# Kernel tuning notes

Measured on AMD Instinct MI355X. Metric: run time of the kernel, lower is better.

The kernel has to match this reference:

```python
import jax, jax.numpy as jnp
import numpy as np

H = 1024        # hidden_units
NH = 16         # num_heads
HD = H // NH    # head_dim = 64
B = 32
S = 500
MAX_SEQ = 500
ROPE_BASE = 10000.0


def setup_inputs() -> dict:
    key = jax.random.key(0)
    ks = jax.random.split(key, 16)
    s = 1.0 / np.sqrt(H)
    inp = {
        "query": jax.random.normal(ks[0], (B, S, H), jnp.float32),
        "key":   jax.random.normal(ks[1], (B, S, H), jnp.float32),
        "value": jax.random.normal(ks[2], (B, S, H), jnp.float32),
        "attn_mask": jax.random.randint(ks[3], (B, S), 0, 2).astype(bool),
        "Wq": jax.random.uniform(ks[4], (H, H), jnp.float32, -s, s),
        "bq": jax.random.uniform(ks[5], (H,), jnp.float32, -s, s),
        "Wk": jax.random.uniform(ks[6], (H, H), jnp.float32, -s, s),
        "bk": jax.random.uniform(ks[7], (H,), jnp.float32, -s, s),
        "Wv": jax.random.uniform(ks[8], (H, H), jnp.float32, -s, s),
        "bv": jax.random.uniform(ks[9], (H,), jnp.float32, -s, s),
        "Wo": jax.random.uniform(ks[10], (H, H), jnp.float32, -s, s),
        "bo": jax.random.uniform(ks[11], (H,), jnp.float32, -s, s),
        # rel_pos_bias embedding table: [2*max_seq_len-1, num_heads]
        "rel_emb": jax.random.normal(ks[12], (2 * MAX_SEQ - 1, NH), jnp.float32),
    }
    return inp


def _rope_tables(seq_len, head_dim, dtype):
    inv_freq = 1.0 / (ROPE_BASE ** (jnp.arange(0, head_dim, 2, dtype=jnp.float32) / head_dim))
    t = jnp.arange(seq_len, dtype=jnp.float32)
    freqs = t[:, None] * inv_freq[None, :]           # [S, HD/2]
    emb = jnp.concatenate([freqs, freqs], axis=-1)   # [S, HD]
    return jnp.cos(emb).astype(dtype), jnp.sin(emb).astype(dtype)


def _apply_rope(x, cos, sin):
    # x: [B, NH, S, HD]; even/odd slicing variant from source
    x_rot = jnp.concatenate([-x[..., 1::2], x[..., 0::2]], axis=-1)
    return x * cos + x_rot * sin


def reference(query, key, value, attn_mask, Wq, bq, Wk, bk, Wv, bv, Wo, bo, rel_emb):
    b, s, _ = query.shape
    Q = (query @ Wq.T + bq).reshape(b, s, NH, HD).transpose(0, 2, 1, 3)  # [B,NH,S,HD]
    K = (key   @ Wk.T + bk).reshape(b, s, NH, HD).transpose(0, 2, 1, 3)
    V = (value @ Wv.T + bv).reshape(b, s, NH, HD).transpose(0, 2, 1, 3)

    cos, sin = _rope_tables(s, HD, Q.dtype)  # [S,HD]
    Q = _apply_rope(Q, cos, sin)
    K = _apply_rope(K, cos, sin)

    # relative-position bias: [1, NH, S, S]
    pos = jnp.arange(s)[:, None] - jnp.arange(s)[None, :]
    rel_idx = jnp.clip(pos + MAX_SEQ - 1, 0, 2 * MAX_SEQ - 2)
    rel_bias = rel_emb[rel_idx].transpose(2, 0, 1)[None]  # [1,NH,S,S]

    # key-padding mask -> additive float mask [B,1,1,S]
    mask_bias = jnp.where(attn_mask[:, None, None, :], 0.0, -jnp.inf).astype(Q.dtype)

    scale = 1.0 / np.sqrt(HD)
    scores = jnp.einsum('bhqd,bhkd->bhqk', Q, K) * scale + mask_bias + rel_bias
    attn = jax.nn.softmax(scores, axis=-1)
    out = jnp.einsum('bhqk,bhkd->bhqd', attn, V)
    out = out.transpose(0, 2, 1, 3).reshape(b, s, H)
    out = jnp.clip(out, -30.0, 30.0)
    return out @ Wo.T + bo
```

## Files before the change

### kernel.cpp

```cpp
#include <hip/hip_runtime.h>
#include <math.h>


typedef unsigned short u16;
typedef unsigned int   u32;
typedef unsigned char  u8;
using bf16x8 = __attribute__((ext_vector_type(8))) short;
using f32x4  = __attribute__((ext_vector_type(4))) float;
using f32x2  = __attribute__((ext_vector_type(2))) float;
using u16x4  = __attribute__((ext_vector_type(4))) unsigned short;

#define DEV __device__ __forceinline__

#if __has_builtin(__builtin_amdgcn_exp2f)
#define EXP2(x) __builtin_amdgcn_exp2f(x)
#else
#define EXP2(x) exp2f(x)
#endif

DEV u16 f2bf(float f) {
  union { float f; u32 u; } c; c.f = f;
  u32 u = c.u;
  return (u16)((u + 0x7FFFu + ((u >> 16) & 1u)) >> 16);
}
DEV float bf2f(u16 h) {
  union { u32 u; float f; } c; c.u = ((u32)h) << 16;
  return c.f;
}
DEV u32 cvtpk(float a, float b) {
  u32 r;
  asm("v_cvt_pk_bf16_f32 %0, %1, %2" : "=v"(r) : "v"(a), "v"(b));
  return r;
}

DEV void async16(void* l, const void* g) {
  __builtin_amdgcn_global_load_lds(
      (__attribute__((address_space(1))) unsigned int*)g,
      (__attribute__((address_space(3))) unsigned int*)l, 16, 0, 0);
}

__global__ __launch_bounds__(512) void build_gather(const void* __restrict__ mraw,
                                                    u16* __restrict__ karr,
                                                    int* __restrict__ kept) {
  const int b = blockIdx.x;
  const int t = threadIdx.x;
  const int lane = t & 63, wave = t >> 6;
  __shared__ int s_li, s_lf;
  __shared__ int wbase[8];
  __shared__ int wpop[8];
  if (t == 0) { s_li = 0; s_lf = 0; }
  __syncthreads();
  const u32* w = (const u32*)mraw;
  int li = 0, lf = 0;
  for (int g = t; g < 4000; g += 512) {
    u32 v = w[g];
    li |= !(v == 0u || v == 1u);
    lf |= !(v == 0u || v == 0x3F800000u);
  }
  if (li) atomicOr(&s_li, 1);
  if (lf) atomicOr(&s_lf, 1);
  __syncthreads();
  const int mode = (!s_li) ? 0 : ((!s_lf) ? 1 : 2);
  int v = 0;
  if (t < 500) {
    if (mode == 0)      v = ((const int*)mraw)[b * 500 + t] != 0;
    else if (mode == 1) v = (((const float*)mraw)[b * 500 + t] != 0.0f);
    else                v = ((const u8*)mraw)[b * 500 + t] != 0;
  }
  unsigned long long bal = __ballot(v != 0);
  karr[b * 512 + t] = 0xFFFF;
  if (lane == 0) wpop[wave] = __popcll(bal);
  __syncthreads();
  if (t == 0) {
    int s = 0;
    for (int ww = 0; ww < 8; ++ww) { wbase[ww] = s; s += wpop[ww]; }
    kept[b] = s;
  }
  __syncthreads();
  if (v) {
    int rank = wbase[wave] + __popcll(bal & ((1ull << lane) - 1ull));
    karr[b * 512 + rank] = (u16)t;
  }
}

__global__ __launch_bounds__(256) void rope_table(float* __restrict__ tab) {
  int idx = blockIdx.x * 256 + threadIdx.x;
  if (idx >= 16000) return;
  int s = idx >> 5, j = idx & 31;
  float ang = (float)s * exp2f(-(float)j * 0.41524100f);
  float sn, cs;
  sincosf(ang, &sn, &cs);
  tab[idx * 2] = cs;
  tab[idx * 2 + 1] = sn;
}

__global__ __launch_bounds__(256) void cvt_w4(const float* __restrict__ w0,
                                              const float* __restrict__ w1,
                                              const float* __restrict__ w2,
                                              const float* __restrict__ w3,
                                              u16* __restrict__ dst) {
  const float* src = (blockIdx.y == 0) ? w0 : (blockIdx.y == 1) ? w1
                    : (blockIdx.y == 2) ? w2 : w3;
  int i = blockIdx.x * 256 + threadIdx.x;
  f32x4 f = *(const f32x4*)(src + (size_t)i * 4);
  u16x4 o;
  o[0] = f2bf(f[0]); o[1] = f2bf(f[1]); o[2] = f2bf(f[2]); o[3] = f2bf(f[3]);
  *(u16x4*)(dst + (size_t)blockIdx.y * 1048576 + (size_t)i * 4) = o;
}

__global__ __launch_bounds__(256) void cvt_f32_bf16(const float* __restrict__ src,
                                                    u16* __restrict__ dst, int n4) {
  int i = blockIdx.x * 256 + threadIdx.x;
  int stride = gridDim.x * 256;
  for (; i < n4; i += stride) {
    f32x4 f = *(const f32x4*)(src + (size_t)i * 4);
    u16x4 o;
    o[0] = f2bf(f[0]); o[1] = f2bf(f[1]); o[2] = f2bf(f[2]); o[3] = f2bf(f[3]);
    *(u16x4*)(dst + (size_t)i * 4) = o;
  }
}

__global__ __launch_bounds__(256) void gathercvt2(const float* __restrict__ srcK,
                                                  const float* __restrict__ srcV,
                                                  const u16* __restrict__ karr,
                                                  const int* __restrict__ kept,
                                                  u16* __restrict__ dstK,
                                                  u16* __restrict__ dstV) {
  const int b = blockIdx.y;
  const int r = blockIdx.x * 2 + (threadIdx.x >> 7);
  if (r >= kept[b]) return;
  const float* src = blockIdx.z ? srcV : srcK;
  u16* dst = blockIdx.z ? dstV : dstK;
  const int c = (threadIdx.x & 127) * 8;
  const int tok = karr[b * 512 + r];
  const float* s = src + ((size_t)b * 500 + tok) * 1024 + c;
  f32x4 f0 = *(const f32x4*)s;
  f32x4 f1 = *(const f32x4*)(s + 4);
  u16 o[8];
  o[0] = f2bf(f0[0]); o[1] = f2bf(f0[1]); o[2] = f2bf(f0[2]); o[3] = f2bf(f0[3]);
  o[4] = f2bf(f1[0]); o[5] = f2bf(f1[1]); o[6] = f2bf(f1[2]); o[7] = f2bf(f1[3]);
  *(bf16x8*)(dst + ((size_t)b * 512 + r) * 1024 + c) = *(bf16x8*)o;
}

template <int MODE>
__global__ __launch_bounds__(512, 4) void gemm_bt(const u16* __restrict__ A,
                                                  const u16* __restrict__ Bw,
                                                  const float* __restrict__ bias,
                                                  void* __restrict__ Cout, int M,
                                                  const float* __restrict__ tabg,
                                                  const int* __restrict__ keptp) {
  const int bid = blockIdx.x;
  int m0, n0, Mloc;
  size_t abase, crowbase;
  if (MODE == 3) {
    const int swz = (bid & 7) * 64 + (bid >> 3);
    const int mb = swz >> 3;
    n0 = (swz & 7) * 128;
    const int b = mb >> 1, rb = mb & 1;
    const int kb = keptp[b];
    if (rb * 256 >= kb) return;
    m0 = rb * 256;
    Mloc = kb;
    abase = (size_t)b * 512 * 1024;
    crowbase = (size_t)b * 512;
  } else {
    const int swz = (bid & 7) * 63 + (bid >> 3);
    m0 = (swz >> 3) * 256;
    n0 = (swz & 7) * 128;
    Mloc = M;
    abase = 0;
    crowbase = 0;
  }
  const int tid = threadIdx.x;
  const int wave = tid >> 6;
  const int wr = wave >> 1, wc = wave & 1;
  const int fr = tid & 15, fo = (tid >> 4) & 3;
  const int fr2 = fr >> 1;
  const int aslot = ((4 * (fr & 1) + fo) ^ fr2) * 8;

  const int ATILE = 128 * 64;
  const int BTILE = 64 * 64;
  __shared__ __attribute__((aligned(16))) u16 AS[2 * 128 * 64];
  __shared__ __attribute__((aligned(16))) u16 BS[2 * 64 * 64];

  f32x4 acc[4][4];
#pragma unroll
  for (int mi = 0; mi < 4; ++mi)
#pragma unroll
    for (int ni = 0; ni < 4; ++ni)
#pragma unroll
      for (int j = 0; j < 4; ++j) acc[mi][ni][j] = 0.f;

  auto STG = [&](int t, int buf) {
    u16* sA = &AS[buf * ATILE];
    u16* sB = &BS[buf * BTILE];
#pragma unroll
    for (int i = 0; i < 2; ++i) {
      int c = i * 512 + tid;
      int r = c >> 3, v = (c & 7) ^ (r & 7);
      int ar = min(m0 + 2 * r + (v >> 2), Mloc - 1);
      async16(&sA[c * 8], A + abase + (size_t)ar * 1024 + t * 32 + (v & 3) * 8);
    }
    {
      int c = tid;
      int r = c >> 3, v = (c & 7) ^ (r & 7);
      int nr = n0 + 2 * r + (v >> 2);
      async16(&sB[c * 8], Bw + (size_t)nr * 1024 + t * 32 + (v & 3) * 8);
    }
  };

  STG(0, 0);
  asm volatile("s_waitcnt vmcnt(0)" ::: "memory");
  __builtin_amdgcn_sched_barrier(0);
  __builtin_amdgcn_s_barrier();

  int cur = 0;
  for (int t = 0; t < 32; ++t) {
    if (t + 1 < 32) STG(t + 1, cur ^ 1);
    const u16* a0 = &AS[cur * ATILE];
    const u16* b0 = &BS[cur * BTILE];
    bf16x8 a[4], b[4];
#pragma unroll
    for (int mi = 0; mi < 4; ++mi)
      a[mi] = *(const bf16x8*)&a0[(wr * 32 + mi * 8 + fr2) * 64 + aslot];
#pragma unroll
    for (int ni = 0; ni < 4; ++ni)
      b[ni] = *(const bf16x8*)&b0[(wc * 32 + ni * 8 + fr2) * 64 + aslot];
    asm volatile("s_waitcnt lgkmcnt(0)" ::: "memory");
    __builtin_amdgcn_sched_barrier(0);
    __builtin_amdgcn_s_setprio(1);
#pragma unroll
    for (int mi = 0; mi < 4; ++mi)
#pragma unroll
      for (int ni = 0; ni < 4; ++ni)
        acc[mi][ni] = __builtin_amdgcn_mfma_f32_16x16x32_bf16(a[mi], b[ni], acc[mi][ni], 0, 0, 0);
    __builtin_amdgcn_s_setprio(0);
    asm volatile("s_waitcnt vmcnt(0)" ::: "memory");
    __builtin_amdgcn_sched_barrier(0);
    __builtin_amdgcn_s_barrier();
    cur ^= 1;
  }

  __syncthreads();
  if (MODE == 2) {
    float* fw = (float*)&AS[0] + wave * 1024;
    const int hh = (n0 >> 6) + wc;
    const int lane = tid & 63;
    const int row = lane >> 2;
    const int jb = (lane & 3) * 8;
    float bvv[4];
#pragma unroll
    for (int ni = 0; ni < 4; ++ni) bvv[ni] = bias[n0 + wc * 64 + ni * 16 + fr];
#pragma unroll
    for (int mi = 0; mi < 4; ++mi) {
#pragma unroll
      for (int ni = 0; ni < 4; ++ni)
#pragma unroll
        for (int r = 0; r < 4; ++r)
          fw[(fo * 4 + r) * 64 + ni * 16 + fr] = acc[mi][ni][r] + bvv[ni];
      int m = m0 + wr * 64 + mi * 16 + row;
      if (m < Mloc) {
        int bb = (u32)m / 500u;
        int ss = m - bb * 500;
        u16* dst = (u16*)Cout + (((size_t)(bb * 16 + hh)) * 500 + ss) * 64;
        bf16x8 va, vb;
#pragma unroll
        for (int p = 0; p < 8; ++p) {
          int j = jb + p;
          float x0 = fw[row * 64 + j];
          float x1 = fw[row * 64 + 32 + j];
          float xe = fw[row * 64 + 2 * j];
          float xo = fw[row * 64 + 2 * j + 1];
          f32x2 cn = *(const f32x2*)(tabg + (ss * 32 + j) * 2);
          va[p] = (short)f2bf(x0 * cn[0] - xo * cn[1]);
          vb[p] = (short)f2bf(x1 * cn[0] + xe * cn[1]);
        }
        *(bf16x8*)(dst + jb) = va;
        *(bf16x8*)(dst + 32 + jb) = vb;
      }
      __builtin_amdgcn_s_barrier();
    }
  } else if (MODE == 1 || MODE == 3) {
    u16* bw = (u16*)&AS[0] + wave * 2048;
#pragma unroll
    for (int mi = 0; mi < 4; ++mi) {
#pragma unroll
      for (int ni = 0; ni < 4; ++ni) {
        float bv = bias[n0 + wc * 64 + ni * 16 + fr];
#pragma unroll
        for (int r = 0; r < 4; ++r)
          bw[(fo * 4 + r) * 64 + ni * 16 + fr] = f2bf(acc[mi][ni][r] + bv);
      }
      int lane = tid & 63;
      int ro = lane >> 2, ch = lane & 3;
      int m = m0 + wr * 64 + mi * 16 + ro;
      bf16x8 v0 = *(const bf16x8*)&bw[ro * 64 + ch * 16];
      bf16x8 v1 = *(const bf16x8*)&bw[ro * 64 + ch * 16 + 8];
      if (m < Mloc) {
        u16* dst = (u16*)Cout + (crowbase + m) * 1024 + n0 + wc * 64 + ch * 16;
        *(bf16x8*)dst = v0;
        *(bf16x8*)(dst + 8) = v1;
      }
    }
  } else {
    float* fw = (float*)&AS[0] + wave * 1024;
#pragma unroll
    for (int mi = 0; mi < 4; ++mi) {
#pragma unroll
      for (int ni = 0; ni < 4; ++ni) {
        float bv = bias[n0 + wc * 64 + ni * 16 + fr];
#pragma unroll
        for (int r = 0; r < 4; ++r)
          fw[(fo * 4 + r) * 64 + ni * 16 + fr] = acc[mi][ni][r] + bv;
      }
      int lane = tid & 63;
      int ro = lane >> 2, ch = lane & 3;
      int m = m0 + wr * 64 + mi * 16 + ro;
      f32x4 v0 = *(const f32x4*)&fw[ro * 64 + ch * 16];
      f32x4 v1 = *(const f32x4*)&fw[ro * 64 + ch * 16 + 4];
      f32x4 v2 = *(const f32x4*)&fw[ro * 64 + ch * 16 + 8];
      f32x4 v3 = *(const f32x4*)&fw[ro * 64 + ch * 16 + 12];
      if (m < Mloc) {
        float* dst = (float*)Cout + (size_t)m * 1024 + n0 + wc * 64 + ch * 16;
        *(f32x4*)dst = v0;
        *(f32x4*)(dst + 4) = v1;
        *(f32x4*)(dst + 8) = v2;
        *(f32x4*)(dst + 12) = v3;
      }
    }
  }
}

__global__ __launch_bounds__(256) void gather_k(const u16* __restrict__ PkC,
                                                const float* __restrict__ tab,
                                                const u16* __restrict__ karr,
                                                const int* __restrict__ kept,
                                                u16* __restrict__ Ktg) {
  const int tile = blockIdx.x;
  const int bh = blockIdx.y;
  const int h = bh & 15, b = bh >> 4;
  if (tile * 64 >= kept[b]) return;
  char* out = (char*)(Ktg + ((size_t)bh * 8 + tile) * 4096);
  const int tid = threadIdx.x;
#pragma unroll
  for (int i = 0; i < 8; ++i) {
    int item = i * 256 + tid;
    int row = item >> 5, j = item & 31;
    int rk = tile * 64 + row;
    int tok = karr[b * 512 + rk];
    int sw = (row & 7) << 4;
    u16 o0 = 0, o1 = 0;
    if (tok != 0xFFFF) {
      const u16* src = PkC + ((size_t)b * 512 + rk) * 1024 + h * 64;
      float x0 = bf2f(src[j]);
      float x1 = bf2f(src[32 + j]);
      float xe = bf2f(src[2 * j]);
      float xo = bf2f(src[2 * j + 1]);
      f32x2 cn = *(const f32x2*)(tab + (tok * 32 + j) * 2);
      o0 = f2bf(x0 * cn[0] - xo * cn[1]);
      o1 = f2bf(x1 * cn[0] + xe * cn[1]);
    }
    *(u16*)(out + row * 128 + ((2 * j) ^ sw)) = o0;
    *(u16*)(out + row * 128 + ((64 + 2 * j) ^ sw)) = o1;
  }
}

__global__ __launch_bounds__(256) void gather_v(const u16* __restrict__ PvC,
                                                const u16* __restrict__ karr,
                                                const int* __restrict__ kept,
                                                u16* __restrict__ Vtg) {
  const int tile = blockIdx.x;
  const int bh = blockIdx.y;
  const int h = bh & 15, b = bh >> 4;
  if (tile * 64 >= kept[b]) return;
  const int tid = threadIdx.x;
  __shared__ __attribute__((aligned(16))) u16 Vl[64 * 64];
#pragma unroll
  for (int i = 0; i < 2; ++i) {
    int chunk = i * 256 + tid;
    int slot = chunk >> 3, seg = chunk & 7;
    int rk = tile * 64 + slot;
    int tok = karr[b * 512 + rk];
    bf16x8 v;
#pragma unroll
    for (int p = 0; p < 8; ++p) v[p] = 0;
    if (tok != 0xFFFF)
      v = *(const bf16x8*)(PvC + ((size_t)b * 512 + rk) * 1024 + h * 64 + seg * 8);
    *(bf16x8*)&Vl[slot * 64 + seg * 8] = v;
  }
  __syncthreads();
  u16* out = Vtg + ((size_t)bh * 8 + tile) * 4096;
#pragma unroll
  for (int i = 0; i < 2; ++i) {
    int chunk = i * 256 + tid;
    int d = chunk >> 3, c16 = chunk & 7;
    int k0 = ((c16 * 16) ^ ((d & 7) << 4)) >> 1;
    bf16x8 v;
#pragma unroll
    for (int p = 0; p < 8; ++p) v[p] = (short)Vl[(k0 + p) * 64 + d];
    *(bf16x8*)(out + chunk * 8) = v;
  }
}

__global__ __launch_bounds__(512) void attn_kernel(const u16* __restrict__ Qr,
                                                   const u16* __restrict__ Ktg,
                                                   const u16* __restrict__ Vtg,
                                                   const float* __restrict__ rel_emb,
                                                   const u16* __restrict__ karr,
                                                   const int* __restrict__ kept,
                                                   u16* __restrict__ AO) {
  const int bid = blockIdx.x;
  const int bh = ((bid >> 5) << 3) | (bid & 7);
  const int qb = (bid >> 3) & 3;
  const int h = bh & 15, b = bh >> 4;
  const int q0 = qb * 128;
  const int tid = threadIdx.x;
  const int wave = tid >> 6;
  const int fr = tid & 15, fo = (tid >> 4) & 3;

  __shared__ __attribute__((aligned(16))) u16 Ks[2][4096];
  __shared__ __attribute__((aligned(16))) u16 Vs[2][4096];
  __shared__ __attribute__((aligned(16))) u16 Pl[8][1024];
  __shared__ float rel2[640];
  __shared__ u16 okk[512];

  const int nt = (kept[b] + 63) >> 6;
  const float LOG2E = 1.44269504f;
  for (int i = tid; i < 640; i += 512) {
    int g = min(max(q0 - 12 + i, 0), 998);
    rel2[i] = (i == 0) ? -1e30f : rel_emb[g * 16 + h] * LOG2E;
  }
  okk[tid] = karr[b * 512 + tid];

  const int qloc = wave * 16 + fr;
  const int qc = qloc + 511;
  const u16* Qb = Qr + ((size_t)bh * 500 + min(q0 + qloc, 499)) * 64;
  bf16x8 qf0 = *(const bf16x8*)(Qb + fo * 8);
  bf16x8 qf1 = *(const bf16x8*)(Qb + 32 + fo * 8);

  f32x4 o[4];
#pragma unroll
  for (int nf = 0; nf < 4; ++nf)
#pragma unroll
    for (int j = 0; j < 4; ++j) o[nf][j] = 0.f;
  float mrun = -1e30f, lrun = 0.f;

  const u16* Kb = Ktg + (size_t)bh * 32768;
  const u16* Vb = Vtg + (size_t)bh * 32768;
  const int sw = (fr & 7) << 4;
  const float SC = 0.18033688f;

  if (nt > 0) {
    async16(&Ks[0][tid * 8], Kb + tid * 8);
    async16(&Vs[0][tid * 8], Vb + tid * 8);
  }
  __syncthreads();

  for (int t = 0; t < nt; ++t) {
    const int cur = t & 1;
    if (t + 1 < nt) {
      async16(&Ks[cur ^ 1][tid * 8], Kb + (t + 1) * 4096 + tid * 8);
      async16(&Vs[cur ^ 1][tid * 8], Vb + (t + 1) * 4096 + tid * 8);
    }
    const char* Kt = (const char*)(cur ? &Ks[1][0] : &Ks[0][0]);
    const char* Vt = (const char*)(cur ? &Vs[1][0] : &Vs[0][0]);

    f32x4 sacc[4];
    __builtin_amdgcn_s_setprio(1);
#pragma unroll
    for (int nf = 0; nf < 4; ++nf) {
#pragma unroll
      for (int jj = 0; jj < 4; ++jj) sacc[nf][jj] = 0.f;
      int rb = (nf * 16 + fr) * 128;
      bf16x8 kb0 = *(const bf16x8*)(Kt + rb + ((fo * 16) ^ sw));
      bf16x8 kb1 = *(const bf16x8*)(Kt + rb + ((64 + fo * 16) ^ sw));
      sacc[nf] = __builtin_amdgcn_mfma_f32_16x16x32_bf16(kb0, qf0, sacc[nf], 0, 0, 0);
      sacc[nf] = __builtin_amdgcn_mfma_f32_16x16x32_bf16(kb1, qf1, sacc[nf], 0, 0, 0);
    }
    __builtin_amdgcn_s_setprio(0);

    float p2[4][4];
    float pmax = -3e30f;
#pragma unroll
    for (int nf = 0; nf < 4; ++nf) {
      u16x4 ok4 = *(const u16x4*)&okk[t * 64 + nf * 16 + fo * 4];
#pragma unroll
      for (int r = 0; r < 4; ++r) {
        int idx2 = max(qc - (int)ok4[r], 0);
        float s2 = fmaf(sacc[nf][r], SC, rel2[idx2]);
        p2[nf][r] = s2;
        pmax = fmaxf(pmax, s2);
      }
    }
    pmax = fmaxf(pmax, __shfl_xor(pmax, 16, 64));
    pmax = fmaxf(pmax, __shfl_xor(pmax, 32, 64));

    if (!__all(pmax <= mrun + 8.0f)) {
      float mnew = fmaxf(mrun, pmax);
      float scl = EXP2(mrun - mnew);
      lrun *= scl;
#pragma unroll
      for (int nf = 0; nf < 4; ++nf)
#pragma unroll
        for (int r = 0; r < 4; ++r) o[nf][r] *= scl;
      mrun = mnew;
    }

    float lsum = 0.f;
#pragma unroll
    for (int nf = 0; nf < 4; ++nf) {
      float e0 = EXP2(p2[nf][0] - mrun);
      float e1 = EXP2(p2[nf][1] - mrun);
      float e2 = EXP2(p2[nf][2] - mrun);
      float e3 = EXP2(p2[nf][3] - mrun);
      lsum += (e0 + e1) + (e2 + e3);
      uint2 w; w.x = cvtpk(e0, e1); w.y = cvtpk(e2, e3);
      *(uint2*)((char*)&Pl[wave][0] + fr * 128 + ((nf * 32 + fo * 8) ^ sw)) = w;
    }
    lsum += __shfl_xor(lsum, 16, 64);
    lsum += __shfl_xor(lsum, 32, 64);
    lrun += lsum;

    bf16x8 pa0 = *(const bf16x8*)((char*)&Pl[wave][0] + fr * 128 + ((fo * 16) ^ sw));
    bf16x8 pa1 = *(const bf16x8*)((char*)&Pl[wave][0] + fr * 128 + ((64 + fo * 16) ^ sw));
    __builtin_amdgcn_s_setprio(1);
#pragma unroll
    for (int nf = 0; nf < 4; ++nf) {
      int rb = (nf * 16 + fr) * 128;
      bf16x8 vb0 = *(const bf16x8*)(Vt + rb + ((fo * 16) ^ sw));
      bf16x8 vb1 = *(const bf16x8*)(Vt + rb + ((64 + fo * 16) ^ sw));
      o[nf] = __builtin_amdgcn_mfma_f32_16x16x32_bf16(vb0, pa0, o[nf], 0, 0, 0);
      o[nf] = __builtin_amdgcn_mfma_f32_16x16x32_bf16(vb1, pa1, o[nf], 0, 0, 0);
    }
    __builtin_amdgcn_s_setprio(0);
    __syncthreads();
  }

  float inv = (lrun > 0.f) ? 1.f / lrun : 0.f;
#pragma unroll
  for (int nf = 0; nf < 4; ++nf) {
    float v0 = fminf(fmaxf(o[nf][0] * inv, -30.f), 30.f);
    float v1 = fminf(fmaxf(o[nf][1] * inv, -30.f), 30.f);
    float v2 = fminf(fmaxf(o[nf][2] * inv, -30.f), 30.f);
    float v3 = fminf(fmaxf(o[nf][3] * inv, -30.f), 30.f);
    uint2 w; w.x = cvtpk(v0, v1); w.y = cvtpk(v2, v3);
    *(uint2*)((char*)&Pl[wave][0] + fr * 128 + ((nf * 32 + fo * 8) ^ sw)) = w;
  }
  {
    int lane = tid & 63;
    int ro = lane >> 2, c = lane & 3;
    int swr = (ro & 7) << 4;
    const char* Pw = (const char*)&Pl[wave][0];
    bf16x8 v0 = *(const bf16x8*)(Pw + ro * 128 + ((c * 32) ^ swr));
    bf16x8 v1 = *(const bf16x8*)(Pw + ro * 128 + ((c * 32 + 16) ^ swr));
    int token = q0 + wave * 16 + ro;
    if (token < 500) {
      u16* dst = AO + (size_t)(b * 500 + token) * 1024 + h * 64 + c * 16;
      *(bf16x8*)dst = v0;
      *(bf16x8*)(dst + 8) = v1;
    }
  }
}

extern "C" void kernel_launch(void* const* d_in, const int* in_sizes, int n_in,
                              void* d_out, int out_size, void* d_ws, size_t ws_size,
                              hipStream_t stream) {
  const float* query = (const float*)d_in[0];
  const float* key_  = (const float*)d_in[1];
  const float* value = (const float*)d_in[2];
  const void*  mask  = d_in[3];
  const float* Wq = (const float*)d_in[4];
  const float* bq = (const float*)d_in[5];
  const float* Wk = (const float*)d_in[6];
  const float* bk = (const float*)d_in[7];
  const float* Wv = (const float*)d_in[8];
  const float* bv = (const float*)d_in[9];
  const float* Wo = (const float*)d_in[10];
  const float* bo = (const float*)d_in[11];
  const float* rel = (const float*)d_in[12];

  char* ws = (char*)d_ws;
  const size_t SLOT = 33554432;
  u16* Wb = (u16*)ws;
  char* Aq = ws + 8388608;
  char* Bq = Aq + SLOT;
  char* Cq = Bq + SLOT;
  char* Dq = Cq + SLOT;
  char* MISC = Dq + SLOT;
  u16* karr  = (u16*)(MISC + 65536);
  int* kept  = (int*)(MISC + 131072);
  float* tab = (float*)(MISC + 131584);

  build_gather<<<32, 512, 0, stream>>>(mask, karr, kept);
  rope_table<<<63, 256, 0, stream>>>(tab);
  cvt_w4<<<dim3(1024, 4), 256, 0, stream>>>(Wq, Wk, Wv, Wo, Wb);
  cvt_f32_bf16<<<2048, 256, 0, stream>>>(query, (u16*)Aq, 4096000);
  gathercvt2<<<dim3(256, 32, 2), 256, 0, stream>>>(key_, value, karr, kept,
                                                   (u16*)Bq, (u16*)Cq);

  gemm_bt<3><<<512, 512, 0, stream>>>((u16*)Cq, Wb + 2 * 1048576, bv, Dq, 0, tab, kept);
  gemm_bt<2><<<504, 512, 0, stream>>>((u16*)Aq, Wb + 0 * 1048576, bq, Cq, 16000, tab, nullptr);
  gemm_bt<3><<<512, 512, 0, stream>>>((u16*)Bq, Wb + 1 * 1048576, bk, Aq, 0, tab, kept);

  gather_k<<<dim3(8, 512), 256, 0, stream>>>((u16*)Aq, tab, karr, kept, (u16*)Bq);
  gather_v<<<dim3(8, 512), 256, 0, stream>>>((u16*)Dq, karr, kept, (u16*)Aq);

  attn_kernel<<<2048, 512, 0, stream>>>((u16*)Cq, (u16*)Bq, (u16*)Aq, rel,
                                        karr, kept, (u16*)Dq);

  gemm_bt<0><<<504, 512, 0, stream>>>((u16*)Dq, Wb + 3 * 1048576, bo, (float*)d_out, 16000, tab, nullptr);
}
```

Measured before the change: 292.0 us.

## Merge Q, K, V projection GEMMs into one launch with block-range dispatch

Replaces three separate projection GEMM launches with one kernel of 1528 blocks. Block index ranges select the Q path (with RoPE epilogue) or the K or V path (compacted rows). The goal is to remove launch gaps and tail underutilisation between the GEMMs so all three share the GPU at once. The Q output is staged in the d_out buffer, which is later overwritten by the output projection, and workspace buffers are reassigned. This only works if d_out is large enough and nothing aliases.

```diff
diff --git a/kernel.cpp b/kernel.cpp
--- a/kernel.cpp
+++ b/kernel.cpp
@@ -142,48 +142,18 @@
   *(bf16x8*)(dst + ((size_t)b * 512 + r) * 1024 + c) = *(bf16x8*)o;
 }
 
-template <int MODE>
-__global__ __launch_bounds__(512, 4) void gemm_bt(const u16* __restrict__ A,
-                                                  const u16* __restrict__ Bw,
-                                                  const float* __restrict__ bias,
-                                                  void* __restrict__ Cout, int M,
-                                                  const float* __restrict__ tabg,
-                                                  const int* __restrict__ keptp) {
-  const int bid = blockIdx.x;
-  int m0, n0, Mloc;
-  size_t abase, crowbase;
-  if (MODE == 3) {
-    const int swz = (bid & 7) * 64 + (bid >> 3);
-    const int mb = swz >> 3;
-    n0 = (swz & 7) * 128;
-    const int b = mb >> 1, rb = mb & 1;
-    const int kb = keptp[b];
-    if (rb * 256 >= kb) return;
-    m0 = rb * 256;
-    Mloc = kb;
-    abase = (size_t)b * 512 * 1024;
-    crowbase = (size_t)b * 512;
-  } else {
-    const int swz = (bid & 7) * 63 + (bid >> 3);
-    m0 = (swz >> 3) * 256;
-    n0 = (swz & 7) * 128;
-    Mloc = M;
-    abase = 0;
-    crowbase = 0;
-  }
-  const int tid = threadIdx.x;
+DEV void gemm_core(const u16* __restrict__ A, size_t abase,
+                   const u16* __restrict__ W,
+                   int m0, int n0, int Mloc,
+                   u16* AS, u16* BS, f32x4 (&acc)[4][4], int tid) {
   const int wave = tid >> 6;
   const int wr = wave >> 1, wc = wave & 1;
   const int fr = tid & 15, fo = (tid >> 4) & 3;
   const int fr2 = fr >> 1;
   const int aslot = ((4 * (fr & 1) + fo) ^ fr2) * 8;
-
   const int ATILE = 128 * 64;
   const int BTILE = 64 * 64;
-  __shared__ __attribute__((aligned(16))) u16 AS[2 * 128 * 64];
-  __shared__ __attribute__((aligned(16))) u16 BS[2 * 64 * 64];
-
-  f32x4 acc[4][4];
+
 #pragma unroll
   for (int mi = 0; mi < 4; ++mi)
 #pragma unroll
@@ -205,7 +175,7 @@
       int c = tid;
       int r = c >> 3, v = (c & 7) ^ (r & 7);
       int nr = n0 + 2 * r + (v >> 2);
-      async16(&sB[c * 8], Bw + (size_t)nr * 1024 + t * 32 + (v & 3) * 8);
+      async16(&sB[c * 8], W + (size_t)nr * 1024 + t * 32 + (v & 3) * 8);
     }
   };
 
@@ -240,9 +210,31 @@
     __builtin_amdgcn_s_barrier();
     cur ^= 1;
   }
-
   __syncthreads();
-  if (MODE == 2) {
+}
+
+__global__ __launch_bounds__(512, 4) void gemm_fused(
+    const u16* __restrict__ Xq, const u16* __restrict__ XkC, const u16* __restrict__ XvC,
+    const u16* __restrict__ Wb,
+    const float* __restrict__ bq, const float* __restrict__ bk, const float* __restrict__ bv,
+    u16* __restrict__ Qro, u16* __restrict__ PkC, u16* __restrict__ PvC,
+    const float* __restrict__ tabg, const int* __restrict__ keptp) {
+  __shared__ __attribute__((aligned(16))) u16 AS[2 * 128 * 64];
+  __shared__ __attribute__((aligned(16))) u16 BS[2 * 64 * 64];
+  const int bid = blockIdx.x;
+  const int tid = threadIdx.x;
+  const int wave = tid >> 6;
+  const int wr = wave >> 1, wc = wave & 1;
+  const int fr = tid & 15, fo = (tid >> 4) & 3;
+
+  f32x4 acc[4][4];
+
+  if (bid < 504) {
+    const int swz = (bid & 7) * 63 + (bid >> 3);
+    const int m0 = (swz >> 3) * 256;
+    const int n0 = (swz & 7) * 128;
+    gemm_core(Xq, 0, Wb, m0, n0, 16000, AS, BS, acc, tid);
+
     float* fw = (float*)&AS[0] + wave * 1024;
     const int hh = (n0 >> 6) + wc;
     const int lane = tid & 63;
@@ -250,7 +242,7 @@
     const int jb = (lane & 3) * 8;
     float bvv[4];
 #pragma unroll
-    for (int ni = 0; ni < 4; ++ni) bvv[ni] = bias[n0 + wc * 64 + ni * 16 + fr];
+    for (int ni = 0; ni < 4; ++ni) bvv[ni] = bq[n0 + wc * 64 + ni * 16 + fr];
 #pragma unroll
     for (int mi = 0; mi < 4; ++mi) {
 #pragma unroll
@@ -259,10 +251,10 @@
         for (int r = 0; r < 4; ++r)
           fw[(fo * 4 + r) * 64 + ni * 16 + fr] = acc[mi][ni][r] + bvv[ni];
       int m = m0 + wr * 64 + mi * 16 + row;
-      if (m < Mloc) {
+      if (m < 16000) {
         int bb = (u32)m / 500u;
         int ss = m - bb * 500;
-        u16* dst = (u16*)Cout + (((size_t)(bb * 16 + hh)) * 500 + ss) * 64;
+        u16* dst = Qro + (((size_t)(bb * 16 + hh)) * 500 + ss) * 64;
         bf16x8 va, vb;
 #pragma unroll
         for (int p = 0; p < 8; ++p) {
@@ -280,53 +272,87 @@
       }
       __builtin_amdgcn_s_barrier();
     }
-  } else if (MODE == 1 || MODE == 3) {
+  } else {
+    const bool isV = (bid >= 1016);
+    const int local = isV ? (bid - 1016) : (bid - 504);
+    const u16* A = isV ? XvC : XkC;
+    const u16* W = Wb + (isV ? 2 : 1) * 1048576;
+    const float* bias = isV ? bv : bk;
+    u16* Cout = isV ? PvC : PkC;
+    const int swz = (local & 7) * 64 + (local >> 3);
+    const int mb = swz >> 3;
+    const int n0 = (swz & 7) * 128;
+    const int b = mb >> 1, rb = mb & 1;
+    const int kb = keptp[b];
+    if (rb * 256 >= kb) return;
+    const int m0 = rb * 256;
+    gemm_core(A, (size_t)b * 512 * 1024, W, m0, n0, kb, AS, BS, acc, tid);
+
     u16* bw = (u16*)&AS[0] + wave * 2048;
 #pragma unroll
     for (int mi = 0; mi < 4; ++mi) {
 #pragma unroll
       for (int ni = 0; ni < 4; ++ni) {
-        float bv = bias[n0 + wc * 64 + ni * 16 + fr];
+        float bvs = bias[n0 + wc * 64 + ni * 16 + fr];
 #pragma unroll
         for (int r = 0; r < 4; ++r)
-          bw[(fo * 4 + r) * 64 + ni * 16 + fr] = f2bf(acc[mi][ni][r] + bv);
+          bw[(fo * 4 + r) * 64 + ni * 16 + fr] = f2bf(acc[mi][ni][r] + bvs);
       }
       int lane = tid & 63;
       int ro = lane >> 2, ch = lane & 3;
       int m = m0 + wr * 64 + mi * 16 + ro;
       bf16x8 v0 = *(const bf16x8*)&bw[ro * 64 + ch * 16];
       bf16x8 v1 = *(const bf16x8*)&bw[ro * 64 + ch * 16 + 8];
-      if (m < Mloc) {
-        u16* dst = (u16*)Cout + (crowbase + m) * 1024 + n0 + wc * 64 + ch * 16;
+      if (m < kb) {
+        u16* dst = Cout + ((size_t)b * 512 + m) * 1024 + n0 + wc * 64 + ch * 16;
         *(bf16x8*)dst = v0;
         *(bf16x8*)(dst + 8) = v1;
       }
     }
-  } else {
-    float* fw = (float*)&AS[0] + wave * 1024;
-#pragma unroll
-    for (int mi = 0; mi < 4; ++mi) {
-#pragma unroll
-      for (int ni = 0; ni < 4; ++ni) {
-        float bv = bias[n0 + wc * 64 + ni * 16 + fr];
-#pragma unroll
-        for (int r = 0; r < 4; ++r)
-          fw[(fo * 4 + r) * 64 + ni * 16 + fr] = acc[mi][ni][r] + bv;
-      }
-      int lane = tid & 63;
-      int ro = lane >> 2, ch = lane & 3;
-      int m = m0 + wr * 64 + mi * 16 + ro;
-      f32x4 v0 = *(const f32x4*)&fw[ro * 64 + ch * 16];
-      f32x4 v1 = *(const f32x4*)&fw[ro * 64 + ch * 16 + 4];
-      f32x4 v2 = *(const f32x4*)&fw[ro * 64 + ch * 16 + 8];
-      f32x4 v3 = *(const f32x4*)&fw[ro * 64 + ch * 16 + 12];
-      if (m < Mloc) {
-        float* dst = (float*)Cout + (size_t)m * 1024 + n0 + wc * 64 + ch * 16;
-        *(f32x4*)dst = v0;
-        *(f32x4*)(dst + 4) = v1;
-        *(f32x4*)(dst + 8) = v2;
-        *(f32x4*)(dst + 12) = v3;
-      }
+  }
+}
+
+__global__ __launch_bounds__(512, 4) void gemm_out(const u16* __restrict__ A,
+                                                   const u16* __restrict__ W,
+                                                   const float* __restrict__ bias,
+                                                   float* __restrict__ Cout) {
+  __shared__ __attribute__((aligned(16))) u16 AS[2 * 128 * 64];
+  __shared__ __attribute__((aligned(16))) u16 BS[2 * 64 * 64];
+  const int bid = blockIdx.x;
+  const int tid = threadIdx.x;
+  const int wave = tid >> 6;
+  const int wr = wave >> 1, wc = wave & 1;
+  const int fr = tid & 15, fo = (tid >> 4) & 3;
+  const int swz = (bid & 7) * 63 + (bid >> 3);
+  const int m0 = (swz >> 3) * 256;
+  const int n0 = (swz & 7) * 128;
+
+  f32x4 acc[4][4];
+  gemm_core(A, 0, W, m0, n0, 16000, AS, BS, acc, tid);
+
+  float* fw = (float*)&AS[0] + wave * 1024;
+#pragma unroll
+  for (int mi = 0; mi < 4; ++mi) {
+#pragma unroll
+    for (int ni = 0; ni < 4; ++ni) {
+      float bv = bias[n0 + wc * 64 + ni * 16 + fr];
+#pragma unroll
+      for (int r = 0; r < 4; ++r)
+        fw[(fo * 4 + r) * 64 + ni * 16 + fr] = acc[mi][ni][r] + bv;
+    }
+    int lane = tid & 63;
+    int ro = lane >> 2, ch = lane & 3;
+    int m = m0 + wr * 64 + mi * 16 + ro;
+    f32x4 v0 = *(const f32x4*)&fw[ro * 64 + ch * 16];
+    f32x4 v1 = *(const f32x4*)&fw[ro * 64 + ch * 16 + 4];
+    f32x4 v2 = *(const f32x4*)&fw[ro * 64 + ch * 16 + 8];
+    f32x4 v3 = *(const f32x4*)&fw[ro * 64 + ch * 16 + 12];
+    if (m < 16000) {
+      float* dst = Cout + (size_t)m * 1024 + n0 + wc * 64 + ch * 16;
+      *(f32x4*)dst = v0;
+      *(f32x4*)(dst + 4) = v1;
+      *(f32x4*)(dst + 8) = v2;
+      *(f32x4*)(dst + 12) = v3;
     }
   }
 }
@@ -586,10 +612,12 @@
   char* Bq = Aq + SLOT;
   char* Cq = Bq + SLOT;
   char* Dq = Cq + SLOT;
-  char* MISC = Dq + SLOT;
+  char* Eq = Dq + SLOT;
+  char* MISC = Eq + SLOT;
   u16* karr  = (u16*)(MISC + 65536);
   int* kept  = (int*)(MISC + 131072);
   float* tab = (float*)(MISC + 131584);
+  u16* Qro = (u16*)d_out;
 
   build_gather<<<32, 512, 0, stream>>>(mask, karr, kept);
   rope_table<<<63, 256, 0, stream>>>(tab);
@@ -598,15 +626,15 @@
   gathercvt2<<<dim3(256, 32, 2), 256, 0, stream>>>(key_, value, karr, kept,
                                                    (u16*)Bq, (u16*)Cq);
 
-  gemm_bt<3><<<512, 512, 0, stream>>>((u16*)Cq, Wb + 2 * 1048576, bv, Dq, 0, tab, kept);
-  gemm_bt<2><<<504, 512, 0, stream>>>((u16*)Aq, Wb + 0 * 1048576, bq, Cq, 16000, tab, nullptr);
-  gemm_bt<3><<<512, 512, 0, stream>>>((u16*)Bq, Wb + 1 * 1048576, bk, Aq, 0, tab, kept);
-
-  gather_k<<<dim3(8, 512), 256, 0, stream>>>((u16*)Aq, tab, karr, kept, (u16*)Bq);
+  gemm_fused<<<1528, 512, 0, stream>>>((u16*)Aq, (u16*)Bq, (u16*)Cq, Wb,
+                                       bq, bk, bv,
+                                       Qro, (u16*)Eq, (u16*)Dq, tab, kept);
+
+  gather_k<<<dim3(8, 512), 256, 0, stream>>>((u16*)Eq, tab, karr, kept, (u16*)Cq);
   gather_v<<<dim3(8, 512), 256, 0, stream>>>((u16*)Dq, karr, kept, (u16*)Aq);
 
-  attn_kernel<<<2048, 512, 0, stream>>>((u16*)Cq, (u16*)Bq, (u16*)Aq, rel,
-                                        karr, kept, (u16*)Dq);
-
-  gemm_bt<0><<<504, 512, 0, stream>>>((u16*)Dq, Wb + 3 * 1048576, bo, (float*)d_out, 16000, tab, nullptr);
-}
+  attn_kernel<<<2048, 512, 0, stream>>>(Qro, (u16*)Cq, (u16*)Aq, rel,
+                                        karr, kept, (u16*)Bq);
+
+  gemm_out<<<504, 512, 0, stream>>>((u16*)Bq, Wb + 3 * 1048576, bo, (float*)d_out);
+}
```

Result: faster. 280.0 us (-4.1%).
